# Kernel tuning notes

Hardware: AMD Instinct MI355X
Metric: run time of the kernel (lower is better)

The kernel has to match this reference:

```python
import jax, jax.numpy as jnp
import numpy as np

N_NODES = 50000
N_EDGES = 800000
UNITS = 64
NUM_RADIAL = 20


def setup_inputs() -> dict:
    key = jax.random.key(0)
    ks = jax.random.split(key, 12)
    u, r = UNITS, NUM_RADIAL
    inv_u = 1.0 / np.sqrt(u)
    inv_r = 1.0 / np.sqrt(r)
    return {
        "node": jax.random.normal(ks[0], (N_NODES, u), jnp.float32),
        "equivariant": jax.random.normal(ks[1], (N_NODES, 3, u), jnp.float32),
        "rbf": jax.random.uniform(ks[2], (N_EDGES, r), jnp.float32),
        "envelope": jax.random.uniform(ks[3], (N_EDGES, 1), jnp.float32),
        "r_ij": jax.random.normal(ks[4], (N_EDGES, 3), jnp.float32),
        "edge_index": jax.random.randint(ks[5], (N_EDGES, 2), 0, N_NODES, jnp.int64),
        "Ws": jax.random.uniform(ks[6], (u, u), jnp.float32, -inv_u, inv_u),
        "bs": jax.random.uniform(ks[7], (u,), jnp.float32, -inv_u, inv_u),
        "Wphi": jax.random.uniform(ks[8], (3 * u, u), jnp.float32, -inv_u, inv_u),
        "bphi": jax.random.uniform(ks[9], (3 * u,), jnp.float32, -inv_u, inv_u),
        "Ww": jax.random.uniform(ks[10], (3 * u, r), jnp.float32, -inv_r, inv_r),
        "bw": jax.random.uniform(ks[11], (3 * u,), jnp.float32, -inv_r, inv_r),
    }


def reference(node, equivariant, rbf, envelope, r_ij, edge_index,
              Ws, bs, Wphi, bphi, Ww, bw):
    n_nodes = node.shape[0]
    u = node.shape[1]
    # per-node dense projections
    s = jax.nn.silu(node @ Ws.T + bs)          # [N, u]
    s = s @ Wphi.T + bphi                      # [N, 3u]
    # gather to edges (source = column 1)
    s_e = s[edge_index[:, 1]]                  # [E, 3u]
    # per-edge radial filter with cutoff envelope
    w = rbf @ Ww.T + bw                        # [E, 3u]
    w = w * envelope
    sw = s_e * w                               # [E, 3u]
    sw1, sw2, sw3 = jnp.split(sw, 3, axis=-1)  # each [E, u]
    dst = edge_index[:, 0]
    ds = jax.ops.segment_sum(sw1, dst, num_segments=n_nodes)  # [N, u]
    vj = equivariant[edge_index[:, 1]]         # [E, 3, u]
    dv = vj * sw2[:, None, :] + r_ij[:, :, None] * sw3[:, None, :]  # [E, 3, u]
    dv = jax.ops.segment_sum(dv, dst, num_segments=n_nodes)   # [N, 3, u]
    return (ds, dv)
```

## Files before the change

### kernel.cpp

```cpp
#include <hip/hip_runtime.h>

#define NRAD 20
#define MNODE 8

__device__ __forceinline__ float rdlane(float v, int l)
{
    return __uint_as_float(__builtin_amdgcn_readlane(__float_as_uint(v), l));
}

__global__ void detect_idx_kernel(const int* __restrict__ eidx, int* __restrict__ flag)
{
    int t = threadIdx.x;
    unsigned long long m = __ballot(eidx[2 * t + 1] != 0);
    if (t == 0) flag[0] = (__popcll(m) > 8) ? 1 : 0;
}

__global__ void hist_kernel(const int* __restrict__ eidx, const int* __restrict__ flag,
                            int* __restrict__ counts, int n_edges)
{
    int fmt32 = flag[0];
    int i0 = blockIdx.x * blockDim.x + threadIdx.x;
    int stride = gridDim.x * blockDim.x;
    if (fmt32) {
        for (int e = i0; e < n_edges; e += stride) atomicAdd(&counts[eidx[2 * e]], 1);
    } else {
        const long long* e64 = (const long long*)eidx;
        for (int e = i0; e < n_edges; e += stride) atomicAdd(&counts[(int)e64[2 * e]], 1);
    }
}

__global__ __launch_bounds__(256)
void scan1_kernel(const int* __restrict__ cnt, int* __restrict__ bsum, int n, int ch)
{
    __shared__ int red[4];
    int b = blockIdx.x, t = threadIdx.x;
    int end = min(n, (b + 1) * ch);
    int v = 0;
    for (int i = b * ch + t; i < end; i += 256) v += cnt[i];
#pragma unroll
    for (int d = 1; d < 64; d <<= 1) v += __shfl_xor(v, d, 64);
    if ((t & 63) == 0) red[t >> 6] = v;
    __syncthreads();
    if (t == 0) bsum[b] = red[0] + red[1] + red[2] + red[3];
}

__global__ __launch_bounds__(256)
void scan2_kernel(const int* __restrict__ bsum, int* __restrict__ bscan,
                  int* __restrict__ offs, int nb, int n)
{
    __shared__ int wsum[4];
    int t = threadIdx.x, lane = t & 63, w = t >> 6;
    int v = (t < nb) ? bsum[t] : 0;
    int sc = v;
#pragma unroll
    for (int d = 1; d < 64; d <<= 1) {
        int u = __shfl_up(sc, (unsigned)d, 64);
        if (lane >= d) sc += u;
    }
    if (lane == 63) wsum[w] = sc;
    __syncthreads();
    int add = 0;
    for (int j = 0; j < w; j++) add += wsum[j];
    int incl = sc + add;
    if (t < nb) bscan[t] = incl - v;
    if (t == nb - 1) offs[n] = incl;
}

__global__ __launch_bounds__(256)
void scan3_kernel(const int* __restrict__ cnt, const int* __restrict__ bscan,
                  int* __restrict__ offs, int* __restrict__ cur, int n, int ch)
{
    __shared__ int wsum[4];
    __shared__ int btot;
    int b = blockIdx.x, t = threadIdx.x, lane = t & 63, w = t >> 6;
    int end = min(n, (b + 1) * ch);
    int carry = bscan[b];
    for (int base = b * ch; base < end; base += 256) {
        int i = base + t;
        int v = (i < end) ? cnt[i] : 0;
        int sc = v;
#pragma unroll
        for (int d = 1; d < 64; d <<= 1) {
            int u = __shfl_up(sc, (unsigned)d, 64);
            if (lane >= d) sc += u;
        }
        if (lane == 63) wsum[w] = sc;
        __syncthreads();
        int add = 0;
        for (int j = 0; j < w; j++) add += wsum[j];
        if (t == 255) btot = sc + add;
        int excl = carry + (sc + add - v);
        if (i < end) { offs[i] = excl; cur[i] = excl; }
        __syncthreads();
        carry += btot;
    }
}

__global__ void scatter_kernel(const int* __restrict__ eidx, const int* __restrict__ flag,
                               int* __restrict__ cur, int* __restrict__ sorted, int n_edges)
{
    int fmt32 = flag[0];
    int i0 = blockIdx.x * blockDim.x + threadIdx.x;
    int stride = gridDim.x * blockDim.x;
    const long long* e64 = (const long long*)eidx;
    for (int e = i0; e < n_edges; e += stride) {
        int dst = fmt32 ? eidx[2 * e] : (int)e64[2 * e];
        int pos = atomicAdd(&cur[dst], 1);
        sorted[pos] = e;
    }
}

__global__ __launch_bounds__(256)
void node_mlp3(const float* __restrict__ node,
               const float* __restrict__ Ws, const float* __restrict__ bs,
               const float* __restrict__ Wphi, const float* __restrict__ bphi,
               float* __restrict__ s_planes, size_t plane_n, int n_nodes)
{
    __shared__ float WsT[64 * 64];
    __shared__ float WphiT[64 * 192];
    const int t = threadIdx.x;
    for (int i = t; i < 64 * 64; i += 256) {
        int j = i >> 6, k = i & 63;
        WsT[k * 64 + j] = Ws[i];
    }
    for (int i = t; i < 192 * 64; i += 256) {
        int j = i >> 6, k = i & 63;
        WphiT[k * 192 + j] = Wphi[i];
    }
    __syncthreads();

    const int lane = t & 63;
    const int wave = t >> 6;
    const int gw = blockIdx.x * 4 + wave;
    const int nw = gridDim.x * 4;
    const float bsc = bs[lane];
    const float bp0 = bphi[lane], bp1 = bphi[64 + lane], bp2 = bphi[128 + lane];
    float* p0 = s_planes;
    float* p1 = s_planes + plane_n;
    float* p2 = s_planes + 2 * plane_n;

    for (int n0 = gw * MNODE; n0 < n_nodes; n0 += nw * MNODE) {
        const int cnt = min(MNODE, n_nodes - n0);
        float x[MNODE];
#pragma unroll
        for (int m = 0; m < MNODE; m++)
            x[m] = (m < cnt) ? node[(size_t)(n0 + m) * 64 + lane] : 0.f;

        float acc[MNODE];
#pragma unroll
        for (int m = 0; m < MNODE; m++) acc[m] = bsc;
#pragma unroll
        for (int k = 0; k < 64; k++) {
            float wv = WsT[k * 64 + lane];
#pragma unroll
            for (int m = 0; m < MNODE; m++) acc[m] += rdlane(x[m], k) * wv;
        }
        float s1[MNODE];
#pragma unroll
        for (int m = 0; m < MNODE; m++) {
            float a = acc[m];
            s1[m] = a / (1.f + __expf(-a));
        }
        float a0[MNODE], a1[MNODE], a2[MNODE];
#pragma unroll
        for (int m = 0; m < MNODE; m++) { a0[m] = bp0; a1[m] = bp1; a2[m] = bp2; }
#pragma unroll
        for (int k = 0; k < 64; k++) {
            float w0 = WphiT[k * 192 + lane];
            float w1 = WphiT[k * 192 + 64 + lane];
            float w2 = WphiT[k * 192 + 128 + lane];
#pragma unroll
            for (int m = 0; m < MNODE; m++) {
                float sv = rdlane(s1[m], k);
                a0[m] += sv * w0;
                a1[m] += sv * w1;
                a2[m] += sv * w2;
            }
        }
#pragma unroll
        for (int m = 0; m < MNODE; m++) {
            if (m < cnt) {
                size_t ob = (size_t)(n0 + m) * 64 + lane;
                p0[ob] = a0[m];
                p1[ob] = a1[m];
                p2[ob] = a2[m];
            }
        }
    }
}

__global__ __launch_bounds__(256)
void accum2_kernel(const float* __restrict__ s_planes, size_t plane_n,
                   const float* __restrict__ eq, const float* __restrict__ rbf,
                   const float* __restrict__ env, const float* __restrict__ rij,
                   const int* __restrict__ eidx, const int* __restrict__ flag,
                   const int* __restrict__ sorted,
                   const float* __restrict__ Ww, const float* __restrict__ bw,
                   float* __restrict__ ds, float* __restrict__ dv,
                   int n_edges)
{
    __shared__ int    sh_dst[4 * 64];
    __shared__ int    sh_src[4 * 64];
    __shared__ float  sh_env[4 * 64];
    __shared__ float  sh_r[4 * 3 * 64];
    __shared__ float4 sh_rbf[4 * 64 * 5];

    const int lane = threadIdx.x & 63;
    const int w = threadIdx.x >> 6;
    const int tile = blockIdx.x * 4 + w;
    const int base = tile * 64;
    const int nvalid = min(64, n_edges - base);
    const int woff = w * 64;

    if (lane < nvalid) {
        int e = sorted[base + lane];
        int d_, s_;
        if (flag[0]) {
            const int2* p2 = (const int2*)eidx;
            int2 v = p2[e];
            d_ = v.x; s_ = v.y;
        } else {
            const longlong2* p2 = (const longlong2*)eidx;
            longlong2 v = p2[e];
            d_ = (int)v.x; s_ = (int)v.y;
        }
        sh_dst[woff + lane] = d_;
        sh_src[woff + lane] = s_;
        sh_env[woff + lane] = env[e];
        sh_r[w * 192 + lane]       = rij[3 * e];
        sh_r[w * 192 + 64 + lane]  = rij[3 * e + 1];
        sh_r[w * 192 + 128 + lane] = rij[3 * e + 2];
        const float4* rbf4 = (const float4*)rbf;
#pragma unroll
        for (int q = 0; q < 5; q++) sh_rbf[(woff + lane) * 5 + q] = rbf4[(size_t)e * 5 + q];
    }
    __syncthreads();

    if (nvalid <= 0) return;

    const float4* Ww4 = (const float4*)Ww;
    float4 w0q[5], w1q[5], w2q[5];
#pragma unroll
    for (int q = 0; q < 5; q++) {
        w0q[q] = Ww4[lane * 5 + q];
        w1q[q] = Ww4[(64 + lane) * 5 + q];
        w2q[q] = Ww4[(128 + lane) * 5 + q];
    }
    const float bw0 = bw[lane], bw1 = bw[64 + lane], bw2 = bw[128 + lane];

    const float* s0p = s_planes;
    const float* s1p = s_planes + plane_n;
    const float* s2p = s_planes + 2 * plane_n;

    float a0 = 0.f, a1 = 0.f, a2 = 0.f, a3 = 0.f;
    int cur = sh_dst[woff];

    for (int j = 0; j < nvalid; j++) {
        int src = sh_src[woff + j];
        float ev = sh_env[woff + j];
        float r0 = sh_r[w * 192 + j];
        float r1 = sh_r[w * 192 + 64 + j];
        float r2 = sh_r[w * 192 + 128 + j];

        float w0 = bw0, w1 = bw1, w2 = bw2;
#pragma unroll
        for (int q = 0; q < 5; q++) {
            float4 rb = sh_rbf[(woff + j) * 5 + q];
            w0 += rb.x * w0q[q].x + rb.y * w0q[q].y + rb.z * w0q[q].z + rb.w * w0q[q].w;
            w1 += rb.x * w1q[q].x + rb.y * w1q[q].y + rb.z * w1q[q].z + rb.w * w1q[q].w;
            w2 += rb.x * w2q[q].x + rb.y * w2q[q].y + rb.z * w2q[q].z + rb.w * w2q[q].w;
        }
        w0 *= ev; w1 *= ev; w2 *= ev;

        size_t sb = (size_t)src * 64 + lane;
        float sw0 = s0p[sb] * w0;
        float sw1 = s1p[sb] * w1;
        float sw2 = s2p[sb] * w2;
        size_t qb = (size_t)src * 192 + lane;
        a0 += sw0;
        a1 += eq[qb] * sw1 + r0 * sw2;
        a2 += eq[qb + 64] * sw1 + r1 * sw2;
        a3 += eq[qb + 128] * sw1 + r2 * sw2;

        int nd = (j + 1 < nvalid) ? sh_dst[woff + j + 1] : -2;
        if (nd != cur) {
            unsafeAtomicAdd(&ds[(size_t)cur * 64 + lane], a0);
            size_t db = (size_t)cur * 192 + lane;
            unsafeAtomicAdd(&dv[db], a1);
            unsafeAtomicAdd(&dv[db + 64], a2);
            unsafeAtomicAdd(&dv[db + 128], a3);
            a0 = a1 = a2 = a3 = 0.f;
            cur = nd;
        }
    }
}

__global__ __launch_bounds__(256, 2)
void node_mlp_kernel(const float* __restrict__ node,
                     const float* __restrict__ Ws,
                     const float* __restrict__ bs,
                     const float* __restrict__ Wphi,
                     const float* __restrict__ bphi,
                     float* __restrict__ s_out,
                     int n_nodes)
{
    __shared__ float WsT[64 * 65];
    __shared__ float WphiT[64 * 193];
    const int t = threadIdx.x;
    for (int i = t; i < 64 * 64; i += 256) {
        int c = i >> 6, k = i & 63;
        WsT[k * 65 + c] = Ws[i];
    }
    for (int i = t; i < 192 * 64; i += 256) {
        int j = i >> 6, k = i & 63;
        WphiT[k * 193 + j] = Wphi[i];
    }
    __syncthreads();

    const int lane = t & 63;
    const int wave = t >> 6;
    const int nwaves = (gridDim.x * blockDim.x) >> 6;
    const float bsc = bs[lane];
    const float bp0 = bphi[lane], bp1 = bphi[64 + lane], bp2 = bphi[128 + lane];

    for (int n = blockIdx.x * 4 + wave; n < n_nodes; n += nwaves) {
        float x = node[(size_t)n * 64 + lane];
        float acc = bsc;
#pragma unroll
        for (int k = 0; k < 64; k++) acc += __shfl(x, k) * WsT[k * 65 + lane];
        float s1 = acc / (1.0f + __expf(-acc));
        float a0 = bp0, a1 = bp1, a2 = bp2;
#pragma unroll
        for (int k = 0; k < 64; k++) {
            float sk = __shfl(s1, k);
            a0 += sk * WphiT[k * 193 + lane];
            a1 += sk * WphiT[k * 193 + 64 + lane];
            a2 += sk * WphiT[k * 193 + 128 + lane];
        }
        size_t ob = (size_t)n * 192;
        s_out[ob + lane] = a0;
        s_out[ob + 64 + lane] = a1;
        s_out[ob + 128 + lane] = a2;
    }
}

__global__ __launch_bounds__(256)
void edge_kernel(const float* __restrict__ s,
                 const float* __restrict__ eq,
                 const float* __restrict__ rbf,
                 const float* __restrict__ env,
                 const float* __restrict__ rij,
                 const int* __restrict__ eidx,
                 const int* __restrict__ idx_flag,
                 const float* __restrict__ Ww,
                 const float* __restrict__ bw,
                 float* __restrict__ ds,
                 float* __restrict__ dv,
                 int n_edges)
{
    const int lane = threadIdx.x & 63;
    const int wglob = (blockIdx.x * blockDim.x + threadIdx.x) >> 6;
    const int nw = (gridDim.x * blockDim.x) >> 6;

    float ww0[NRAD], ww1[NRAD], ww2[NRAD];
#pragma unroll
    for (int k = 0; k < NRAD; k++) {
        ww0[k] = Ww[lane * NRAD + k];
        ww1[k] = Ww[(64 + lane) * NRAD + k];
        ww2[k] = Ww[(128 + lane) * NRAD + k];
    }
    const float bw0 = bw[lane], bw1 = bw[64 + lane], bw2 = bw[128 + lane];
    const int fmt32 = idx_flag[0];

    for (int e = wglob; e < n_edges; e += nw) {
        int dst, src;
        if (fmt32) {
            dst = eidx[2 * e];
            src = eidx[2 * e + 1];
        } else {
            const long long* e64 = (const long long*)eidx;
            dst = (int)e64[2 * e];
            src = (int)e64[2 * e + 1];
        }
        float ev = env[e];
        float r0 = rij[3 * e], r1 = rij[3 * e + 1], r2 = rij[3 * e + 2];
        float rb[NRAD];
#pragma unroll
        for (int k = 0; k < NRAD; k++) rb[k] = rbf[(size_t)e * NRAD + k];
        float w0 = bw0, w1 = bw1, w2 = bw2;
#pragma unroll
        for (int k = 0; k < NRAD; k++) {
            w0 += rb[k] * ww0[k];
            w1 += rb[k] * ww1[k];
            w2 += rb[k] * ww2[k];
        }
        w0 *= ev; w1 *= ev; w2 *= ev;

        size_t sb = (size_t)src * 192;
        float sw0 = s[sb + lane] * w0;
        float sw1 = s[sb + 64 + lane] * w1;
        float sw2 = s[sb + 128 + lane] * w2;
        float v0 = eq[sb + lane];
        float v1 = eq[sb + 64 + lane];
        float v2 = eq[sb + 128 + lane];

        unsafeAtomicAdd(&ds[(size_t)dst * 64 + lane], sw0);
        size_t db = (size_t)dst * 192;
        unsafeAtomicAdd(&dv[db + lane],       v0 * sw1 + r0 * sw2);
        unsafeAtomicAdd(&dv[db + 64 + lane],  v1 * sw1 + r1 * sw2);
        unsafeAtomicAdd(&dv[db + 128 + lane], v2 * sw1 + r2 * sw2);
    }
}

extern "C" void kernel_launch(void* const* d_in, const int* in_sizes, int n_in,
                              void* d_out, int out_size, void* d_ws, size_t ws_size,
                              hipStream_t stream)
{
    const float* node = (const float*)d_in[0];
    const float* eq   = (const float*)d_in[1];
    const float* rbf  = (const float*)d_in[2];
    const float* env  = (const float*)d_in[3];
    const float* rij  = (const float*)d_in[4];
    const int*   eidx = (const int*)d_in[5];
    const float* Ws   = (const float*)d_in[6];
    const float* bs   = (const float*)d_in[7];
    const float* Wphi = (const float*)d_in[8];
    const float* bphi = (const float*)d_in[9];
    const float* Ww   = (const float*)d_in[10];
    const float* bw   = (const float*)d_in[11];

    const int n_nodes = in_sizes[0] / 64;
    const int n_edges = in_sizes[3];

    float* out = (float*)d_out;
    float* ds = out;
    float* dv = out + (size_t)n_nodes * 64;

    size_t off = 0;
    auto alloc = [&](size_t bytes) { size_t o = off; off = (off + bytes + 255) & ~(size_t)255; return o; };
    const size_t plane_n = (size_t)n_nodes * 64;
    size_t o_planes = alloc(3 * plane_n * sizeof(float));
    size_t o_cnt    = alloc(2 * (size_t)n_nodes * sizeof(int));
    size_t o_offs   = alloc(((size_t)n_nodes + 1) * sizeof(int));
    size_t o_sorted = alloc((size_t)n_edges * sizeof(int));
    size_t o_bsum   = alloc(512 * sizeof(int));
    size_t o_flag   = alloc(16);
    size_t needed = off;

    char* ws = (char*)d_ws;

    if (ws_size >= needed) {
        float* s_planes = (float*)(ws + o_planes);
        int*   counts   = (int*)(ws + o_cnt);
        int*   cur      = counts + n_nodes;
        int*   offs     = (int*)(ws + o_offs);
        int*   sorted   = (int*)(ws + o_sorted);
        int*   bsum     = (int*)(ws + o_bsum);
        int*   bscan    = bsum + 256;
        int*   flag     = (int*)(ws + o_flag);

        const int ch = (n_nodes + 255) / 256;
        const int nb = (n_nodes + ch - 1) / ch;

        hipMemsetAsync(counts, 0, (size_t)n_nodes * sizeof(int), stream);
        hipMemsetAsync(d_out, 0, (size_t)out_size * sizeof(float), stream);
        detect_idx_kernel<<<1, 64, 0, stream>>>(eidx, flag);
        hist_kernel<<<1024, 256, 0, stream>>>(eidx, flag, counts, n_edges);
        scan1_kernel<<<nb, 256, 0, stream>>>(counts, bsum, n_nodes, ch);
        scan2_kernel<<<1, 256, 0, stream>>>(bsum, bscan, offs, nb, n_nodes);
        scan3_kernel<<<nb, 256, 0, stream>>>(counts, bscan, offs, cur, n_nodes, ch);
        scatter_kernel<<<1024, 256, 0, stream>>>(eidx, flag, cur, sorted, n_edges);
        node_mlp3<<<512, 256, 0, stream>>>(node, Ws, bs, Wphi, bphi,
                                           s_planes, plane_n, n_nodes);
        const int n_tiles = (n_edges + 63) / 64;
        accum2_kernel<<<(n_tiles + 3) / 4, 256, 0, stream>>>(
            s_planes, plane_n, eq, rbf, env, rij, eidx, flag, sorted,
            Ww, bw, ds, dv, n_edges);
    } else {
        float* s_ws = (float*)d_ws;
        int* idx_flag = (int*)(ws + (size_t)n_nodes * 192 * sizeof(float));
        hipMemsetAsync(d_out, 0, (size_t)out_size * sizeof(float), stream);
        detect_idx_kernel<<<1, 64, 0, stream>>>(eidx, idx_flag);
        node_mlp_kernel<<<1024, 256, 0, stream>>>(node, Ws, bs, Wphi, bphi, s_ws, n_nodes);
        edge_kernel<<<4096, 256, 0, stream>>>(s_ws, eq, rbf, env, rij, eidx, idx_flag,
                                              Ww, bw, ds, dv, n_edges);
    }
}
```

Measured before the change: 613.1 us.

## Store node features in bf16 planes and pre-sort packed edge records

Node projections and equivariant features are now stored as bf16 planes, which halves the bytes moved by the random per-edge gathers. The scatter step also writes a packed 64-byte record per edge in sorted order: src, dst, envelope, r_ij and the rbf values as bf16. The accumulate kernel then reads edge data contiguously instead of indirectly through a sorted index. The cost is an extra cast pass over eq, a larger scatter write, and lower precision of intermediates that may breach tolerance.

```diff
diff --git a/kernel.cpp b/kernel.cpp
--- a/kernel.cpp
+++ b/kernel.cpp
@@ -3,10 +3,29 @@
 #define NRAD 20
 #define MNODE 8
 
+typedef unsigned short ushort_t;
+typedef unsigned int uint_t;
+
 __device__ __forceinline__ float rdlane(float v, int l)
 {
     return __uint_as_float(__builtin_amdgcn_readlane(__float_as_uint(v), l));
 }
+
+__device__ __forceinline__ ushort_t f2bf(float f)
+{
+    uint_t u = __float_as_uint(f);
+    u += 0x7fff + ((u >> 16) & 1);
+    return (ushort_t)(u >> 16);
+}
+
+__device__ __forceinline__ uint_t pack2bf(float a, float b)
+{
+    return (uint_t)f2bf(a) | ((uint_t)f2bf(b) << 16);
+}
+
+__device__ __forceinline__ float bflo(uint_t w) { return __uint_as_float(w << 16); }
+__device__ __forceinline__ float bfhi(uint_t w) { return __uint_as_float(w & 0xffff0000u); }
+__device__ __forceinline__ float bf2f(ushort_t h) { return __uint_as_float(((uint_t)h) << 16); }
 
 __global__ void detect_idx_kernel(const int* __restrict__ eidx, int* __restrict__ flag)
 {
@@ -45,8 +64,7 @@
 }
 
 __global__ __launch_bounds__(256)
-void scan2_kernel(const int* __restrict__ bsum, int* __restrict__ bscan,
-                  int* __restrict__ offs, int nb, int n)
+void scan2_kernel(const int* __restrict__ bsum, int* __restrict__ bscan, int nb)
 {
     __shared__ int wsum[4];
     int t = threadIdx.x, lane = t & 63, w = t >> 6;
@@ -61,14 +79,12 @@
     __syncthreads();
     int add = 0;
     for (int j = 0; j < w; j++) add += wsum[j];
-    int incl = sc + add;
-    if (t < nb) bscan[t] = incl - v;
-    if (t == nb - 1) offs[n] = incl;
+    if (t < nb) bscan[t] = (sc + add) - v;
 }
 
 __global__ __launch_bounds__(256)
 void scan3_kernel(const int* __restrict__ cnt, const int* __restrict__ bscan,
-                  int* __restrict__ offs, int* __restrict__ cur, int n, int ch)
+                  int* __restrict__ cur, int n, int ch)
 {
     __shared__ int wsum[4];
     __shared__ int btot;
@@ -90,9 +106,46 @@
         for (int j = 0; j < w; j++) add += wsum[j];
         if (t == 255) btot = sc + add;
         int excl = carry + (sc + add - v);
-        if (i < end) { offs[i] = excl; cur[i] = excl; }
+        if (i < end) cur[i] = excl;
         __syncthreads();
         carry += btot;
+    }
+}
+
+__global__ void scatter_rec_kernel(const int* __restrict__ eidx, const int* __restrict__ flag,
+                                   int* __restrict__ cur,
+                                   const float* __restrict__ env, const float* __restrict__ rij,
+                                   const float* __restrict__ rbf,
+                                   uint4* __restrict__ rec, int n_edges)
+{
+    int fmt32 = flag[0];
+    int i0 = blockIdx.x * blockDim.x + threadIdx.x;
+    int stride = gridDim.x * blockDim.x;
+    const long long* e64 = (const long long*)eidx;
+    const float4* rbf4 = (const float4*)rbf;
+    for (int e = i0; e < n_edges; e += stride) {
+        int dst, src;
+        if (fmt32) { dst = eidx[2 * e]; src = eidx[2 * e + 1]; }
+        else       { dst = (int)e64[2 * e]; src = (int)e64[2 * e + 1]; }
+        int pos = atomicAdd(&cur[dst], 1);
+        float ev = env[e];
+        float r0 = rij[3 * e], r1 = rij[3 * e + 1], r2 = rij[3 * e + 2];
+        float4 b0 = rbf4[(size_t)e * 5 + 0];
+        float4 b1 = rbf4[(size_t)e * 5 + 1];
+        float4 b2 = rbf4[(size_t)e * 5 + 2];
+        float4 b3 = rbf4[(size_t)e * 5 + 3];
+        float4 b4 = rbf4[(size_t)e * 5 + 4];
+        uint4 qa, qb, qc, qd;
+        qa.x = (uint_t)src; qa.y = (uint_t)dst;
+        qa.z = __float_as_uint(ev); qa.w = __float_as_uint(r0);
+        qb.x = __float_as_uint(r1); qb.y = __float_as_uint(r2);
+        qb.z = pack2bf(b0.x, b0.y); qb.w = pack2bf(b0.z, b0.w);
+        qc.x = pack2bf(b1.x, b1.y); qc.y = pack2bf(b1.z, b1.w);
+        qc.z = pack2bf(b2.x, b2.y); qc.w = pack2bf(b2.z, b2.w);
+        qd.x = pack2bf(b3.x, b3.y); qd.y = pack2bf(b3.z, b3.w);
+        qd.z = pack2bf(b4.x, b4.y); qd.w = pack2bf(b4.z, b4.w);
+        size_t rp = (size_t)pos * 4;
+        rec[rp] = qa; rec[rp + 1] = qb; rec[rp + 2] = qc; rec[rp + 3] = qd;
     }
 }
 
@@ -110,11 +163,29 @@
     }
 }
 
+__global__ void eq_cast_kernel(const float* __restrict__ eq,
+                               ushort_t* __restrict__ p0, ushort_t* __restrict__ p1,
+                               ushort_t* __restrict__ p2, int n_nodes)
+{
+    int i0 = blockIdx.x * blockDim.x + threadIdx.x;
+    int stride = gridDim.x * blockDim.x;
+    int total = n_nodes * 192;
+    for (int i = i0; i < total; i += stride) {
+        int n = i / 192;
+        int r = i - n * 192;
+        int c = r >> 6, ch = r & 63;
+        ushort_t v = f2bf(eq[i]);
+        ushort_t* p = (c == 0) ? p0 : (c == 1) ? p1 : p2;
+        p[(size_t)n * 64 + ch] = v;
+    }
+}
+
 __global__ __launch_bounds__(256)
-void node_mlp3(const float* __restrict__ node,
-               const float* __restrict__ Ws, const float* __restrict__ bs,
-               const float* __restrict__ Wphi, const float* __restrict__ bphi,
-               float* __restrict__ s_planes, size_t plane_n, int n_nodes)
+void node_mlp3b(const float* __restrict__ node,
+                const float* __restrict__ Ws, const float* __restrict__ bs,
+                const float* __restrict__ Wphi, const float* __restrict__ bphi,
+                ushort_t* __restrict__ p0, ushort_t* __restrict__ p1,
+                ushort_t* __restrict__ p2, int n_nodes)
 {
     __shared__ float WsT[64 * 64];
     __shared__ float WphiT[64 * 192];
@@ -135,9 +206,6 @@
     const int nw = gridDim.x * 4;
     const float bsc = bs[lane];
     const float bp0 = bphi[lane], bp1 = bphi[64 + lane], bp2 = bphi[128 + lane];
-    float* p0 = s_planes;
-    float* p1 = s_planes + plane_n;
-    float* p2 = s_planes + 2 * plane_n;
 
     for (int n0 = gw * MNODE; n0 < n_nodes; n0 += nw * MNODE) {
         const int cnt = min(MNODE, n_nodes - n0);
@@ -181,23 +249,26 @@
         for (int m = 0; m < MNODE; m++) {
             if (m < cnt) {
                 size_t ob = (size_t)(n0 + m) * 64 + lane;
-                p0[ob] = a0[m];
-                p1[ob] = a1[m];
-                p2[ob] = a2[m];
+                p0[ob] = f2bf(a0[m]);
+                p1[ob] = f2bf(a1[m]);
+                p2[ob] = f2bf(a2[m]);
             }
         }
     }
 }
 
+template <bool USE_REC>
 __global__ __launch_bounds__(256)
-void accum2_kernel(const float* __restrict__ s_planes, size_t plane_n,
-                   const float* __restrict__ eq, const float* __restrict__ rbf,
-                   const float* __restrict__ env, const float* __restrict__ rij,
-                   const int* __restrict__ eidx, const int* __restrict__ flag,
-                   const int* __restrict__ sorted,
+void accum3_kernel(const ushort_t* __restrict__ s0p, const ushort_t* __restrict__ s1p,
+                   const ushort_t* __restrict__ s2p,
+                   const ushort_t* __restrict__ q0p, const ushort_t* __restrict__ q1p,
+                   const ushort_t* __restrict__ q2p,
+                   const uint4* __restrict__ rec,
+                   const float* __restrict__ rbf, const float* __restrict__ env,
+                   const float* __restrict__ rij, const int* __restrict__ eidx,
+                   const int* __restrict__ flag, const int* __restrict__ sorted,
                    const float* __restrict__ Ww, const float* __restrict__ bw,
-                   float* __restrict__ ds, float* __restrict__ dv,
-                   int n_edges)
+                   float* __restrict__ ds, float* __restrict__ dv, int n_edges)
 {
     __shared__ int    sh_dst[4 * 64];
     __shared__ int    sh_src[4 * 64];
@@ -213,26 +284,43 @@
     const int woff = w * 64;
 
     if (lane < nvalid) {
-        int e = sorted[base + lane];
-        int d_, s_;
-        if (flag[0]) {
-            const int2* p2 = (const int2*)eidx;
-            int2 v = p2[e];
-            d_ = v.x; s_ = v.y;
+        if (USE_REC) {
+            size_t rp = (size_t)(base + lane) * 4;
+            uint4 qa = rec[rp], qb = rec[rp + 1], qc = rec[rp + 2], qd = rec[rp + 3];
+            sh_src[woff + lane] = (int)qa.x;
+            sh_dst[woff + lane] = (int)qa.y;
+            sh_env[woff + lane] = __uint_as_float(qa.z);
+            sh_r[w * 192 + lane]       = __uint_as_float(qa.w);
+            sh_r[w * 192 + 64 + lane]  = __uint_as_float(qb.x);
+            sh_r[w * 192 + 128 + lane] = __uint_as_float(qb.y);
+            float4* dstq = &sh_rbf[(woff + lane) * 5];
+            dstq[0] = make_float4(bflo(qb.z), bfhi(qb.z), bflo(qb.w), bfhi(qb.w));
+            dstq[1] = make_float4(bflo(qc.x), bfhi(qc.x), bflo(qc.y), bfhi(qc.y));
+            dstq[2] = make_float4(bflo(qc.z), bfhi(qc.z), bflo(qc.w), bfhi(qc.w));
+            dstq[3] = make_float4(bflo(qd.x), bfhi(qd.x), bflo(qd.y), bfhi(qd.y));
+            dstq[4] = make_float4(bflo(qd.z), bfhi(qd.z), bflo(qd.w), bfhi(qd.w));
         } else {
-            const longlong2* p2 = (const longlong2*)eidx;
-            longlong2 v = p2[e];
-            d_ = (int)v.x; s_ = (int)v.y;
-        }
-        sh_dst[woff + lane] = d_;
-        sh_src[woff + lane] = s_;
-        sh_env[woff + lane] = env[e];
-        sh_r[w * 192 + lane]       = rij[3 * e];
-        sh_r[w * 192 + 64 + lane]  = rij[3 * e + 1];
-        sh_r[w * 192 + 128 + lane] = rij[3 * e + 2];
-        const float4* rbf4 = (const float4*)rbf;
-#pragma unroll
-        for (int q = 0; q < 5; q++) sh_rbf[(woff + lane) * 5 + q] = rbf4[(size_t)e * 5 + q];
+            int e = sorted[base + lane];
+            int d_, s_;
+            if (flag[0]) {
+                const int2* p2 = (const int2*)eidx;
+                int2 v = p2[e];
+                d_ = v.x; s_ = v.y;
+            } else {
+                const longlong2* p2 = (const longlong2*)eidx;
+                longlong2 v = p2[e];
+                d_ = (int)v.x; s_ = (int)v.y;
+            }
+            sh_dst[woff + lane] = d_;
+            sh_src[woff + lane] = s_;
+            sh_env[woff + lane] = env[e];
+            sh_r[w * 192 + lane]       = rij[3 * e];
+            sh_r[w * 192 + 64 + lane]  = rij[3 * e + 1];
+            sh_r[w * 192 + 128 + lane] = rij[3 * e + 2];
+            const float4* rbf4 = (const float4*)rbf;
+#pragma unroll
+            for (int q = 0; q < 5; q++) sh_rbf[(woff + lane) * 5 + q] = rbf4[(size_t)e * 5 + q];
+        }
     }
     __syncthreads();
 
@@ -247,10 +335,6 @@
         w2q[q] = Ww4[(128 + lane) * 5 + q];
     }
     const float bw0 = bw[lane], bw1 = bw[64 + lane], bw2 = bw[128 + lane];
-
-    const float* s0p = s_planes;
-    const float* s1p = s_planes + plane_n;
-    const float* s2p = s_planes + 2 * plane_n;
 
     float a0 = 0.f, a1 = 0.f, a2 = 0.f, a3 = 0.f;
     int cur = sh_dst[woff];
@@ -262,6 +346,14 @@
         float r1 = sh_r[w * 192 + 64 + j];
         float r2 = sh_r[w * 192 + 128 + j];
 
+        size_t sb = (size_t)src * 64 + lane;
+        float sv0 = bf2f(s0p[sb]);
+        float sv1 = bf2f(s1p[sb]);
+        float sv2 = bf2f(s2p[sb]);
+        float v0 = bf2f(q0p[sb]);
+        float v1 = bf2f(q1p[sb]);
+        float v2 = bf2f(q2p[sb]);
+
         float w0 = bw0, w1 = bw1, w2 = bw2;
 #pragma unroll
         for (int q = 0; q < 5; q++) {
@@ -272,15 +364,12 @@
         }
         w0 *= ev; w1 *= ev; w2 *= ev;
 
-        size_t sb = (size_t)src * 64 + lane;
-        float sw0 = s0p[sb] * w0;
-        float sw1 = s1p[sb] * w1;
-        float sw2 = s2p[sb] * w2;
-        size_t qb = (size_t)src * 192 + lane;
-        a0 += sw0;
-        a1 += eq[qb] * sw1 + r0 * sw2;
-        a2 += eq[qb + 64] * sw1 + r1 * sw2;
-        a3 += eq[qb + 128] * sw1 + r2 * sw2;
+        float sw1 = sv1 * w1;
+        float sw2 = sv2 * w2;
+        a0 += sv0 * w0;
+        a1 += v0 * sw1 + r0 * sw2;
+        a2 += v1 * sw1 + r1 * sw2;
+        a3 += v2 * sw1 + r2 * sw2;
 
         int nd = (j + 1 < nvalid) ? sh_dst[woff + j + 1] : -2;
         if (nd != cur) {
@@ -435,48 +524,96 @@
     float* out = (float*)d_out;
     float* ds = out;
     float* dv = out + (size_t)n_nodes * 64;
-
-    size_t off = 0;
-    auto alloc = [&](size_t bytes) { size_t o = off; off = (off + bytes + 255) & ~(size_t)255; return o; };
+    char* ws = (char*)d_ws;
+
     const size_t plane_n = (size_t)n_nodes * 64;
-    size_t o_planes = alloc(3 * plane_n * sizeof(float));
-    size_t o_cnt    = alloc(2 * (size_t)n_nodes * sizeof(int));
-    size_t o_offs   = alloc(((size_t)n_nodes + 1) * sizeof(int));
-    size_t o_sorted = alloc((size_t)n_edges * sizeof(int));
-    size_t o_bsum   = alloc(512 * sizeof(int));
-    size_t o_flag   = alloc(16);
-    size_t needed = off;
-
-    char* ws = (char*)d_ws;
-
-    if (ws_size >= needed) {
-        float* s_planes = (float*)(ws + o_planes);
-        int*   counts   = (int*)(ws + o_cnt);
-        int*   cur      = counts + n_nodes;
-        int*   offs     = (int*)(ws + o_offs);
-        int*   sorted   = (int*)(ws + o_sorted);
-        int*   bsum     = (int*)(ws + o_bsum);
-        int*   bscan    = bsum + 256;
-        int*   flag     = (int*)(ws + o_flag);
-
-        const int ch = (n_nodes + 255) / 256;
-        const int nb = (n_nodes + ch - 1) / ch;
-
-        hipMemsetAsync(counts, 0, (size_t)n_nodes * sizeof(int), stream);
-        hipMemsetAsync(d_out, 0, (size_t)out_size * sizeof(float), stream);
-        detect_idx_kernel<<<1, 64, 0, stream>>>(eidx, flag);
-        hist_kernel<<<1024, 256, 0, stream>>>(eidx, flag, counts, n_edges);
-        scan1_kernel<<<nb, 256, 0, stream>>>(counts, bsum, n_nodes, ch);
-        scan2_kernel<<<1, 256, 0, stream>>>(bsum, bscan, offs, nb, n_nodes);
-        scan3_kernel<<<nb, 256, 0, stream>>>(counts, bscan, offs, cur, n_nodes, ch);
-        scatter_kernel<<<1024, 256, 0, stream>>>(eidx, flag, cur, sorted, n_edges);
-        node_mlp3<<<512, 256, 0, stream>>>(node, Ws, bs, Wphi, bphi,
-                                           s_planes, plane_n, n_nodes);
-        const int n_tiles = (n_edges + 63) / 64;
-        accum2_kernel<<<(n_tiles + 3) / 4, 256, 0, stream>>>(
-            s_planes, plane_n, eq, rbf, env, rij, eidx, flag, sorted,
-            Ww, bw, ds, dv, n_edges);
-    } else {
+    const int ch = (n_nodes + 255) / 256;
+    const int nb = (n_nodes + ch - 1) / ch;
+
+    {
+        size_t off = 0;
+        auto alloc = [&](size_t bytes) { size_t o = off; off = (off + bytes + 255) & ~(size_t)255; return o; };
+        size_t o_sp   = alloc(3 * plane_n * sizeof(ushort_t));
+        size_t o_qp   = alloc(3 * plane_n * sizeof(ushort_t));
+        size_t o_cnt  = alloc(2 * (size_t)n_nodes * sizeof(int));
+        size_t o_rec  = alloc((size_t)n_edges * 64);
+        size_t o_bsum = alloc(512 * sizeof(int));
+        size_t o_flag = alloc(16);
+        if (ws_size >= off) {
+            ushort_t* sp = (ushort_t*)(ws + o_sp);
+            ushort_t* qp = (ushort_t*)(ws + o_qp);
+            int* counts = (int*)(ws + o_cnt);
+            int* cur = counts + n_nodes;
+            uint4* rec = (uint4*)(ws + o_rec);
+            int* bsum = (int*)(ws + o_bsum);
+            int* bscan = bsum + 256;
+            int* flag = (int*)(ws + o_flag);
+
+            hipMemsetAsync(counts, 0, (size_t)n_nodes * sizeof(int), stream);
+            hipMemsetAsync(d_out, 0, (size_t)out_size * sizeof(float), stream);
+            detect_idx_kernel<<<1, 64, 0, stream>>>(eidx, flag);
+            hist_kernel<<<1024, 256, 0, stream>>>(eidx, flag, counts, n_edges);
+            scan1_kernel<<<nb, 256, 0, stream>>>(counts, bsum, n_nodes, ch);
+            scan2_kernel<<<1, 256, 0, stream>>>(bsum, bscan, nb);
+            scan3_kernel<<<nb, 256, 0, stream>>>(counts, bscan, cur, n_nodes, ch);
+            scatter_rec_kernel<<<1024, 256, 0, stream>>>(eidx, flag, cur, env, rij, rbf,
+                                                         rec, n_edges);
+            eq_cast_kernel<<<1024, 256, 0, stream>>>(eq, qp, qp + plane_n, qp + 2 * plane_n,
+                                                     n_nodes);
+            node_mlp3b<<<512, 256, 0, stream>>>(node, Ws, bs, Wphi, bphi,
+                                                sp, sp + plane_n, sp + 2 * plane_n, n_nodes);
+            const int n_tiles = (n_edges + 63) / 64;
+            accum3_kernel<true><<<(n_tiles + 3) / 4, 256, 0, stream>>>(
+                sp, sp + plane_n, sp + 2 * plane_n,
+                qp, qp + plane_n, qp + 2 * plane_n,
+                rec, rbf, env, rij, eidx, flag, (const int*)nullptr,
+                Ww, bw, ds, dv, n_edges);
+            return;
+        }
+    }
+
+    {
+        size_t off = 0;
+        auto alloc = [&](size_t bytes) { size_t o = off; off = (off + bytes + 255) & ~(size_t)255; return o; };
+        size_t o_sp   = alloc(3 * plane_n * sizeof(ushort_t));
+        size_t o_qp   = alloc(3 * plane_n * sizeof(ushort_t));
+        size_t o_cnt  = alloc(2 * (size_t)n_nodes * sizeof(int));
+        size_t o_sort = alloc((size_t)n_edges * sizeof(int));
+        size_t o_bsum = alloc(512 * sizeof(int));
+        size_t o_flag = alloc(16);
+        if (ws_size >= off) {
+            ushort_t* sp = (ushort_t*)(ws + o_sp);
+            ushort_t* qp = (ushort_t*)(ws + o_qp);
+            int* counts = (int*)(ws + o_cnt);
+            int* cur = counts + n_nodes;
+            int* sorted = (int*)(ws + o_sort);
+            int* bsum = (int*)(ws + o_bsum);
+            int* bscan = bsum + 256;
+            int* flag = (int*)(ws + o_flag);
+
+            hipMemsetAsync(counts, 0, (size_t)n_nodes * sizeof(int), stream);
+            hipMemsetAsync(d_out, 0, (size_t)out_size * sizeof(float), stream);
+            detect_idx_kernel<<<1, 64, 0, stream>>>(eidx, flag);
+            hist_kernel<<<1024, 256, 0, stream>>>(eidx, flag, counts, n_edges);
+            scan1_kernel<<<nb, 256, 0, stream>>>(counts, bsum, n_nodes, ch);
+            scan2_kernel<<<1, 256, 0, stream>>>(bsum, bscan, nb);
+            scan3_kernel<<<nb, 256, 0, stream>>>(counts, bscan, cur, n_nodes, ch);
+            scatter_kernel<<<1024, 256, 0, stream>>>(eidx, flag, cur, sorted, n_edges);
+            eq_cast_kernel<<<1024, 256, 0, stream>>>(eq, qp, qp + plane_n, qp + 2 * plane_n,
+                                                     n_nodes);
+            node_mlp3b<<<512, 256, 0, stream>>>(node, Ws, bs, Wphi, bphi,
+                                                sp, sp + plane_n, sp + 2 * plane_n, n_nodes);
+            const int n_tiles = (n_edges + 63) / 64;
+            accum3_kernel<false><<<(n_tiles + 3) / 4, 256, 0, stream>>>(
+                sp, sp + plane_n, sp + 2 * plane_n,
+                qp, qp + plane_n, qp + 2 * plane_n,
+                (const uint4*)nullptr, rbf, env, rij, eidx, flag, sorted,
+                Ww, bw, ds, dv, n_edges);
+            return;
+        }
+    }
+
+    {
         float* s_ws = (float*)d_ws;
         int* idx_flag = (int*)(ws + (size_t)n_nodes * 192 * sizeof(float));
         hipMemsetAsync(d_out, 0, (size_t)out_size * sizeof(float), stream);
```

Result: faster. 598.2 us (-2.4%).
